# Kernel optimization log

Measured on AMD Instinct MI355X. Metric: run time of the kernel, lower is better.

Reference implementation:

```python
import jax, jax.numpy as jnp
import numpy as np
from jax import lax

B, CIN, COUT, H, W = 4, 256, 256, 64, 64
K, DG, STRIDE, PAD, DIL = 3, 1, 1, 1, 1
K2 = K * K
CG = CIN // DG
HO = (H + 2 * PAD - DIL * (K - 1) - 1) // STRIDE + 1
WO = (W + 2 * PAD - DIL * (K - 1) - 1) // STRIDE + 1


def setup_inputs() -> dict:
    key = jax.random.key(0)
    k1, k2, k3 = jax.random.split(key, 3)
    inputs = jax.random.normal(k1, (B, CIN, H, W), jnp.float32)
    # original init_offset() zeros these; small random weights instead so offsets ~0.5px
    w_off = jax.random.normal(k2, (3 * DG * K2, CIN, K, K), jnp.float32) * 0.01
    b_off = jnp.zeros((3 * DG * K2,), jnp.float32)
    w_dcn = jax.random.normal(k3, (COUT, CIN, K, K), jnp.float32) * (1.0 / np.sqrt(CIN * K2))
    b_dcn = jnp.zeros((COUT,), jnp.float32)
    return {"inputs": inputs, "w_off": w_off, "b_off": b_off, "w_dcn": w_dcn, "b_dcn": b_dcn}


def _conv2d(x, w, b):
    y = lax.conv_general_dilated(x, w, (STRIDE, STRIDE), [(PAD, PAD), (PAD, PAD)],
                                 rhs_dilation=(DIL, DIL),
                                 dimension_numbers=("NCHW", "OIHW", "NCHW"))
    return y + b[None, :, None, None]


def _dcn_forward(inputs, w_off, b_off, w_dcn, b_dcn):
    # offset/mask branch (standard conv), then chunk into o1, o2, mask
    om = _conv2d(inputs, w_off, b_off)                      # [B, 3*DG*K2, HO, WO]
    o1, o2, m = jnp.split(om, 3, axis=1)
    offset = jnp.concatenate([o1, o2], axis=1)              # [B, 2*DG*K2, HO, WO]
    mask = jax.nn.sigmoid(m)                                # [B, DG*K2, HO, WO]

    # DCNv2 offset layout: per deformable group, K2 taps of (dy, dx)
    off = offset.reshape(B, DG, K2, 2, HO, WO)
    dy, dx = off[:, :, :, 0], off[:, :, :, 1]               # [B, DG, K2, HO, WO]

    taps = jnp.arange(K2)
    ki = (taps // K).astype(jnp.float32)
    kj = (taps % K).astype(jnp.float32)
    hb = (jnp.arange(HO, dtype=jnp.float32) * STRIDE - PAD)
    wb = (jnp.arange(WO, dtype=jnp.float32) * STRIDE - PAD)
    py = dy + hb[None, None, None, :, None] + (ki * DIL)[None, None, :, None, None]
    px = dx + wb[None, None, None, None, :] + (kj * DIL)[None, None, :, None, None]

    y0f, x0f = jnp.floor(py), jnp.floor(px)
    ly, lx = py - y0f, px - x0f
    y0, x0 = y0f.astype(jnp.int32), x0f.astype(jnp.int32)
    y1, x1 = y0 + 1, x0 + 1

    flat = inputs.reshape(B, DG, CG, H * W)

    def corner(yi, xi, wgt):
        valid = (yi >= 0) & (yi < H) & (xi >= 0) & (xi < W)
        yc = jnp.clip(yi, 0, H - 1)
        xc = jnp.clip(xi, 0, W - 1)
        idx = (yc * W + xc).reshape(B, DG, 1, K2 * HO * WO)
        idx = jnp.broadcast_to(idx, (B, DG, CG, K2 * HO * WO))
        v = jnp.take_along_axis(flat, idx, axis=3).reshape(B, DG, CG, K2, HO, WO)
        w = jnp.where(valid, wgt, 0.0)[:, :, None]          # zero outside (zero-pad bilinear)
        return v * w

    val = (corner(y0, x0, (1 - ly) * (1 - lx)) + corner(y0, x1, (1 - ly) * lx)
           + corner(y1, x0, ly * (1 - lx)) + corner(y1, x1, ly * lx))

    cols = val * mask.reshape(B, DG, 1, K2, HO, WO)         # modulated columns
    cols = cols.reshape(B, CIN * K2, HO * WO)
    out = jnp.einsum("ok,bkn->bon", w_dcn.reshape(COUT, CIN * K2), cols)
    out = out + b_dcn[None, :, None]
    return out.reshape(B, COUT, HO, WO)


def reference(inputs, w_off, b_off, w_dcn, b_dcn):
    return _dcn_forward(inputs, w_off, b_off, w_dcn, b_dcn)
```

## Files before the change

### kernel.cpp

```cpp
#include <hip/hip_runtime.h>
#include <hip/hip_bf16.h>

typedef __bf16 bf16x8 __attribute__((ext_vector_type(8)));
typedef __bf16 bf16x4 __attribute__((ext_vector_type(4)));
typedef float f32x4 __attribute__((ext_vector_type(4)));
typedef unsigned int u32x4 __attribute__((ext_vector_type(4)));

#define CIN 256
#define COUT 256
#define KDIM 2304

__device__ __forceinline__ void gload_lds16(const void* g, void* l) {
  __builtin_amdgcn_global_load_lds(
      (__attribute__((address_space(1))) unsigned int*)g,
      (__attribute__((address_space(3))) unsigned int*)l, 16, 0, 0);
}

__global__ __launch_bounds__(256) void k_prep_all(const float* __restrict__ wdcn,
                                                  const float* __restrict__ woff,
                                                  const float* __restrict__ in,
                                                  __bf16* __restrict__ Ag,
                                                  __bf16* __restrict__ Ah,
                                                  __bf16* __restrict__ inT) {
  int bid = blockIdx.x, tid = threadIdx.x;
  if (bid < 288) {
    int t8 = bid * 256 + tid;
    int cout = t8 / 288;
    int r8 = t8 - cout * 288;
    int tap = r8 >> 5;
    int cin0 = (r8 & 31) << 3;
    bf16x8 vv;
#pragma unroll
    for (int j = 0; j < 8; ++j)
      vv[j] = (__bf16)wdcn[(cout * 256 + cin0 + j) * 9 + tap];
    *(bf16x8*)&Ag[t8 << 3] = vv;
  } else if (bid < 324) {
    int t8 = (bid - 288) * 256 + tid;
    int l = t8 & 63;
    int mh = (t8 >> 6) & 1;
    int s = t8 >> 7;
    int tap = s >> 3, cc = s & 7;
    int ki = tap / 3, kj = tap - ki * 3;
    int oc = mh * 16 + (l & 15);
    int cinb = cc * 32 + ((l >> 4) << 3);
    bf16x8 hv;
#pragma unroll
    for (int j = 0; j < 8; ++j) {
      float v = (oc < 27) ? woff[((oc * 256 + cinb + j) * 3 + ki) * 3 + kj] : 0.f;
      hv[j] = (__bf16)v;
    }
    *(bf16x8*)&Ah[t8 << 3] = hv;
  } else {
    int idx = bid - 324;
    int h = idx & 63, b = idx >> 6;
    int c = tid;
    const float* src = in + ((((b << 8) + c) << 6) + h) * 64;
    __bf16* dst = inT + (((b << 12) + (h << 6)) << 8) + c;
#pragma unroll
    for (int w4 = 0; w4 < 16; ++w4) {
      f32x4 v = *(const f32x4*)(src + (w4 << 2));
#pragma unroll
      for (int k = 0; k < 4; ++k) dst[(((w4 << 2) + k)) << 8] = (__bf16)v[k];
    }
  }
}

__global__ __launch_bounds__(256) void k_conv(const __bf16* __restrict__ inT,
                                              const __bf16* __restrict__ Ah,
                                              float* __restrict__ omp) {
  __shared__ __bf16 xh[3 * 4 * 66 * 8];
  __shared__ __bf16 sW[9 * 1024];
  int tid = threadIdx.x;
  int l = tid & 63, wn = tid >> 6;
  int ho = blockIdx.x, b = blockIdx.y, ct = blockIdx.z;

  f32x4 acc[2];
  acc[0] = (f32x4){0.f, 0.f, 0.f, 0.f};
  acc[1] = (f32x4){0.f, 0.f, 0.f, 0.f};

  for (int chunk = 0; chunk < 4; ++chunk) {
    int cin0 = ct * 128 + chunk * 32;
    int scc = ct * 4 + chunk;
    u32x4* sW4 = (u32x4*)sW;
#pragma unroll
    for (int i = 0; i < 5; ++i) {
      int s = i * 256 + tid;
      if (s < 1152) {
        int tap = s >> 7, w = s & 127;
        const __bf16* src = Ah + (((tap * 8 + scc) * 2) << 9) + (w << 3);
        gload_lds16((const void*)src, (void*)&sW4[i * 256 + (tid & ~63)]);
      }
    }
    for (int i = tid; i < 792; i += 256) {
      int c = i % 66;
      int t2 = i / 66;
      int u = t2 & 3, r = t2 >> 2;
      int h = ho - 1 + r, w = c - 1;
      bool ok = ((unsigned)h < 64u) & ((unsigned)w < 64u);
      bf16x8 hv = (bf16x8){};
      if (ok)
        hv = *(const bf16x8*)(inT + ((((b << 12) + (h << 6) + w)) << 8) + cin0 +
                              (u << 3));
      *(bf16x8*)&xh[((r * 4 + u) * 66 + c) << 3] = hv;
    }
    __syncthreads();
#pragma unroll
    for (int tap = 0; tap < 9; ++tap) {
      int ki = tap / 3, kj = tap - ki * 3;
      bf16x8 ah0 = *(const bf16x8*)&sW[tap * 1024 + (l << 3)];
      bf16x8 ah1 = *(const bf16x8*)&sW[tap * 1024 + 512 + (l << 3)];
      int u = l >> 4;
      int sc = (wn << 4) + (l & 15) + kj;
      bf16x8 bh = *(const bf16x8*)&xh[((ki * 4 + u) * 66 + sc) << 3];
      acc[0] = __builtin_amdgcn_mfma_f32_16x16x32_bf16(ah0, bh, acc[0], 0, 0, 0);
      acc[1] = __builtin_amdgcn_mfma_f32_16x16x32_bf16(ah1, bh, acc[1], 0, 0, 0);
    }
    __syncthreads();
  }
  int n = (ho << 6) + (wn << 4) + (l & 15);
#pragma unroll
  for (int mh = 0; mh < 2; ++mh)
#pragma unroll
    for (int r = 0; r < 4; ++r) {
      int oc = mh * 16 + ((l >> 4) << 2) + r;
      if (oc < 27)
        omp[(((ct * 4 + b) * 27 + oc) << 12) + n] = acc[mh][r];
    }
}

__global__ __launch_bounds__(512, 4) void k_gemm(const __bf16* __restrict__ inT,
                                                 const float* __restrict__ omp,
                                                 const float* __restrict__ boff,
                                                 const __bf16* __restrict__ Ag,
                                                 const float* __restrict__ bdcn,
                                                 float* __restrict__ out) {
  __shared__ u32x4 sA[2048];
  __shared__ u32x4 sB[256];
  int tid = threadIdx.x;
  int l = tid & 63;
  int w = tid >> 6;
  int wm = w & 3, wh = w >> 2;
  int id = blockIdx.x;
  int x = id & 7, t = id >> 3;
  int b = x >> 1;
  int ntile = ((x & 1) << 6) + t;
  int sn = tid >> 4;
  int sc = tid & 15;
  int n_g = (ntile << 5) + sn;
  const __bf16* tb = inT + ((b << 12) << 8);

  f32x4 acc[4];
#pragma unroll
  for (int i = 0; i < 4; ++i) acc[i] = (f32x4){0.f, 0.f, 0.f, 0.f};

  float w00 = 0.f, w01 = 0.f, w10 = 0.f, w11 = 0.f;
  int o00 = 0, o01 = 0, o10 = 0, o11 = 0;
  bf16x4 cA, cB, cC, cD;
  u32x4 ar[4];

  auto do_corners = [&](int tap) {
    int ki = tap / 3, kj = tap - ki * 3;
    float dy = omp[((b * 27 + 2 * tap) << 12) + n_g] +
               omp[(((4 + b) * 27 + 2 * tap) << 12) + n_g] + boff[2 * tap];
    float dx = omp[((b * 27 + 2 * tap + 1) << 12) + n_g] +
               omp[(((4 + b) * 27 + 2 * tap + 1) << 12) + n_g] + boff[2 * tap + 1];
    float mv = omp[((b * 27 + 18 + tap) << 12) + n_g] +
               omp[(((4 + b) * 27 + 18 + tap) << 12) + n_g] + boff[18 + tap];
    float msk = 1.f / (1.f + __expf(-mv));
    float py = dy + (float)((n_g >> 6) - 1 + ki);
    float px = dx + (float)((n_g & 63) - 1 + kj);
    float y0f = floorf(py), x0f = floorf(px);
    float ly = py - y0f, lx = px - x0f;
    int y0 = (int)y0f, x0 = (int)x0f;
    int y1 = y0 + 1, x1 = x0 + 1;
    bool vy0 = (y0 >= 0) & (y0 < 64), vy1 = (y1 >= 0) & (y1 < 64);
    bool vx0 = (x0 >= 0) & (x0 < 64), vx1 = (x1 >= 0) & (x1 < 64);
    float hy = 1.f - ly, hx = 1.f - lx;
    w00 = (vy0 & vx0) ? hy * hx * msk : 0.f;
    w01 = (vy0 & vx1) ? hy * lx * msk : 0.f;
    w10 = (vy1 & vx0) ? ly * hx * msk : 0.f;
    w11 = (vy1 & vx1) ? ly * lx * msk : 0.f;
    int y0c = min(max(y0, 0), 63), y1c = min(max(y1, 0), 63);
    int x0c = min(max(x0, 0), 63), x1c = min(max(x1, 0), 63);
    o00 = (y0c << 6) + x0c;
    o01 = (y0c << 6) + x1c;
    o10 = (y1c << 6) + x0c;
    o11 = (y1c << 6) + x1c;
  };
  auto do_gather = [&](int s1) {
    int cb0 = ((s1 & 3) << 6) + (sc << 2);
    cA = *(const bf16x4*)(tb + (o00 << 8) + cb0);
    cB = *(const bf16x4*)(tb + (o01 << 8) + cb0);
    cC = *(const bf16x4*)(tb + (o10 << 8) + cb0);
    cD = *(const bf16x4*)(tb + (o11 << 8) + cb0);
  };
  auto do_aload = [&](int s1) {
    int kk0 = s1 << 6;
#pragma unroll
    for (int i = 0; i < 4; ++i) {
      int slot = i * 512 + tid;
      int m = slot >> 3, j = slot & 7;
      int csrc = j ^ (m & 7);
      ar[i] = *(const u32x4*)(Ag + m * KDIM + kk0 + (csrc << 3));
    }
  };

  do_corners(0);
  do_gather(0);
  do_aload(0);

  for (int step = 0; step < 36; ++step) {
    bf16x4 vv;
#pragma unroll
    for (int j = 0; j < 4; ++j) {
      vv[j] = (__bf16)(w00 * (float)cA[j] + w01 * (float)cB[j] +
                       w10 * (float)cC[j] + w11 * (float)cD[j]);
    }
    __syncthreads();
#pragma unroll
    for (int i = 0; i < 4; ++i) sA[i * 512 + tid] = ar[i];
    {
      unsigned long long* sB64 = (unsigned long long*)sB;
      int slot = (sn << 3) + ((sc >> 1) ^ (sn & 7));
      sB64[slot * 2 + (sc & 1)] = __builtin_bit_cast(unsigned long long, vv);
    }
    __syncthreads();
    if (step < 35) {
      int s1 = step + 1;
      if ((s1 & 3) == 0) do_corners(s1 >> 2);
      do_gather(s1);
      do_aload(s1);
    }
#pragma unroll
    for (int kt = 0; kt < 2; ++kt) {
      bf16x8 af[4], bfr;
      int cc = (kt << 2) + (l >> 4);
#pragma unroll
      for (int mf = 0; mf < 4; ++mf) {
        int m = (wm << 6) + (mf << 4) + (l & 15);
        af[mf] = __builtin_bit_cast(bf16x8, sA[(m << 3) + (cc ^ (m & 7))]);
      }
      {
        int n = (wh << 4) + (l & 15);
        bfr = __builtin_bit_cast(bf16x8, sB[(n << 3) + (cc ^ (n & 7))]);
      }
#pragma unroll
      for (int mf = 0; mf < 4; ++mf)
        acc[mf] = __builtin_amdgcn_mfma_f32_16x16x32_bf16(af[mf], bfr, acc[mf],
                                                          0, 0, 0);
    }
  }
#pragma unroll
  for (int mf = 0; mf < 4; ++mf)
#pragma unroll
    for (int r = 0; r < 4; ++r) {
      int m = (wm << 6) + (mf << 4) + ((l >> 4) << 2) + r;
      int n = (ntile << 5) + (wh << 4) + (l & 15);
      out[((b * COUT + m) << 12) + n] = acc[mf][r] + bdcn[m];
    }
}

extern "C" void kernel_launch(void* const* d_in, const int* in_sizes, int n_in,
                              void* d_out, int out_size, void* d_ws, size_t ws_size,
                              hipStream_t stream) {
  const float* in = (const float*)d_in[0];
  const float* woff = (const float*)d_in[1];
  const float* boff = (const float*)d_in[2];
  const float* wdcn = (const float*)d_in[3];
  const float* bdcn = (const float*)d_in[4];
  float* out = (float*)d_out;
  char* ws = (char*)d_ws;
  __bf16* Ag = (__bf16*)ws;
  __bf16* Ah = (__bf16*)(ws + 1179648);
  float* omp = (float*)(ws + 1474560);
  __bf16* inT = (__bf16*)(ws + 5013504);
  k_prep_all<<<580, 256, 0, stream>>>(wdcn, woff, in, Ag, Ah, inT);
  k_conv<<<dim3(64, 4, 2), 256, 0, stream>>>(inT, Ah, omp);
  k_gemm<<<512, 512, 0, stream>>>(inT, omp, boff, Ag, bdcn, out);
}
```

Measured before the change: 79.16 us.

## Double-buffer LDS and stream weight tiles with direct global-to-LDS loads

Replaces the register-staged load-then-store of weight tiles with global_load_lds DMA straight into shared memory. The A and B tiles are now double-buffered so the fetch for step s+2 overlaps the MFMA work of step s, and the barriers become a manual lgkmcnt wait plus s_barrier. This targets the register pressure and the per-step LDS store traffic of the old staging path. In exchange, LDS use doubles to about 72KB per block, which cuts the number of resident 512-thread blocks. Also, global_load_lds completion is counted by vmcnt, not lgkmcnt, so the sync may depend on compiler-inserted vmcnt waits to stay correct.

```diff
diff --git a/kernel.cpp b/kernel.cpp
--- a/kernel.cpp
+++ b/kernel.cpp
@@ -134,8 +134,8 @@
                                                  const __bf16* __restrict__ Ag,
                                                  const float* __restrict__ bdcn,
                                                  float* __restrict__ out) {
-  __shared__ u32x4 sA[2048];
-  __shared__ u32x4 sB[256];
+  __shared__ u32x4 sA[2][2048];
+  __shared__ u32x4 sB[2][256];
   int tid = threadIdx.x;
   int l = tid & 63;
   int w = tid >> 6;
@@ -156,7 +156,6 @@
   float w00 = 0.f, w01 = 0.f, w10 = 0.f, w11 = 0.f;
   int o00 = 0, o01 = 0, o10 = 0, o11 = 0;
   bf16x4 cA, cB, cC, cD;
-  u32x4 ar[4];
 
   auto do_corners = [&](int tap) {
     int ki = tap / 3, kj = tap - ki * 3;
@@ -194,43 +193,46 @@
     cC = *(const bf16x4*)(tb + (o10 << 8) + cb0);
     cD = *(const bf16x4*)(tb + (o11 << 8) + cb0);
   };
-  auto do_aload = [&](int s1) {
+  auto dma_A = [&](int s1, int buf) {
     int kk0 = s1 << 6;
 #pragma unroll
     for (int i = 0; i < 4; ++i) {
       int slot = i * 512 + tid;
       int m = slot >> 3, j = slot & 7;
       int csrc = j ^ (m & 7);
-      ar[i] = *(const u32x4*)(Ag + m * KDIM + kk0 + (csrc << 3));
-    }
+      const __bf16* src = Ag + m * KDIM + kk0 + (csrc << 3);
+      gload_lds16((const void*)src, (void*)&sA[buf][i * 512 + (tid & ~63)]);
+    }
+  };
+  auto barrier_lgkm = [&]() {
+    asm volatile("s_waitcnt lgkmcnt(0)" ::: "memory");
+    __builtin_amdgcn_s_barrier();
   };
 
   do_corners(0);
+  dma_A(0, 0);
   do_gather(0);
-  do_aload(0);
-
-  for (int step = 0; step < 36; ++step) {
+  dma_A(1, 1);
+
+  for (int s = 0; s < 36; ++s) {
     bf16x4 vv;
 #pragma unroll
     for (int j = 0; j < 4; ++j) {
       vv[j] = (__bf16)(w00 * (float)cA[j] + w01 * (float)cB[j] +
                        w10 * (float)cC[j] + w11 * (float)cD[j]);
     }
-    __syncthreads();
-#pragma unroll
-    for (int i = 0; i < 4; ++i) sA[i * 512 + tid] = ar[i];
     {
-      unsigned long long* sB64 = (unsigned long long*)sB;
+      unsigned long long* sB64 = (unsigned long long*)&sB[s & 1][0];
       int slot = (sn << 3) + ((sc >> 1) ^ (sn & 7));
       sB64[slot * 2 + (sc & 1)] = __builtin_bit_cast(unsigned long long, vv);
     }
-    __syncthreads();
-    if (step < 35) {
-      int s1 = step + 1;
+    if (s < 35) {
+      int s1 = s + 1;
       if ((s1 & 3) == 0) do_corners(s1 >> 2);
       do_gather(s1);
-      do_aload(s1);
-    }
+    }
+    barrier_lgkm();
+    int pb = s & 1;
 #pragma unroll
     for (int kt = 0; kt < 2; ++kt) {
       bf16x8 af[4], bfr;
@@ -238,18 +240,21 @@
 #pragma unroll
       for (int mf = 0; mf < 4; ++mf) {
         int m = (wm << 6) + (mf << 4) + (l & 15);
-        af[mf] = __builtin_bit_cast(bf16x8, sA[(m << 3) + (cc ^ (m & 7))]);
+        af[mf] = __builtin_bit_cast(bf16x8, sA[pb][(m << 3) + (cc ^ (m & 7))]);
       }
       {
         int n = (wh << 4) + (l & 15);
-        bfr = __builtin_bit_cast(bf16x8, sB[(n << 3) + (cc ^ (n & 7))]);
+        bfr = __builtin_bit_cast(bf16x8, sB[pb][(n << 3) + (cc ^ (n & 7))]);
       }
 #pragma unroll
       for (int mf = 0; mf < 4; ++mf)
         acc[mf] = __builtin_amdgcn_mfma_f32_16x16x32_bf16(af[mf], bfr, acc[mf],
                                                           0, 0, 0);
     }
+    barrier_lgkm();
+    if (s < 34) dma_A(s + 2, s & 1);
   }
+
 #pragma unroll
   for (int mf = 0; mf < 4; ++mf)
 #pragma unroll
```

Result: faster. 77.39 us (-2.2%).
